# Optimization experiments

Hardware: AMD Instinct MI355X
Metric: run time of the kernel (lower is better)

The kernel has to match this reference:

```python
import jax, jax.numpy as jnp
import numpy as np

_H = jnp.array([[1, 1, 1, 1], [1, -1, 1, -1], [1, 1, -1, -1], [1, -1, -1, 1]], dtype=jnp.float32)
_H2 = _H[jnp.array([1, 0, 2, 3]), :]
_IH = 0.25 * _H[1:3, :]    # inverse Hadamard (H/4), rows 1:3 as in source
_IH2 = 0.25 * _H2[1:3, :]
K = 4  # kernel
S = 2  # stride


def setup_inputs() -> dict:
    key = jax.random.key(0)
    k1, k2, k3 = jax.random.split(key, 3)
    x = jax.random.normal(k1, (32, 64, 56, 56), dtype=jnp.float32)
    weight = jax.random.normal(k2, (128, 64, 4, 4), dtype=jnp.float32) * 0.05
    bias = jax.random.normal(k3, (1, 128, 1, 1), dtype=jnp.float32) * 0.05
    return {"x": x, "weight": weight, "bias": bias}


def reference(x, weight, bias):
    N, C, ih, iw = x.shape
    OC = weight.shape[0]
    nH, nW = ih // S, iw // S  # tiles after stride-2 unfold of the padded input
    xp = jnp.pad(x, ((0, 0), (0, 0), (1, 1), (1, 1)))
    # patches[n,c,h,w,a,b]: a = width-window index, b = height-window index
    # (matches torch x.unfold(3,K,S).unfold(2,K,S) dim ordering)
    patches = jnp.stack(
        [jnp.stack([xp[:, :, bb:bb + 2 * nH:S, aa:aa + 2 * nW:S] for bb in range(K)], axis=-1)
         for aa in range(K)], axis=-2)  # (N,C,nH,nW,K,K)
    # forward Hadamard transforms:  H @ p @ H   and   H2^T @ p @ H2
    T1 = jnp.einsum('ia,nchwab,bj->nchwij', _H, patches, _H)
    T2 = jnp.einsum('ai,nchwab,bj->nchwij', _H2, patches, _H2)
    half = OC // 2
    # elementwise multiply in transform domain + sum over input channels (vectorized over o)
    y1 = jnp.einsum('nchwij,ocij->nohwij', T1, weight[:half])
    y2 = jnp.einsum('nchwij,ocij->nohwij', T2, weight[half:])
    # inverse transform: IH @ y @ IH^T -> 2x2 output tiles
    z1 = jnp.einsum('pi,nohwij,qj->nohwpq', _IH, y1, _IH)
    z2 = jnp.einsum('pi,nohwij,qj->nohwpq', _IH2, y2, _IH2)
    hm = jnp.concatenate([z1, z2], axis=1)  # (N,OC,nH,nW,2,2)
    out = hm.transpose(0, 1, 2, 4, 3, 5).reshape(N, OC, ih, iw)
    return out + bias
```

## Files before the change

### kernel.cpp

```cpp
#include <hip/hip_runtime.h>

typedef __attribute__((ext_vector_type(8))) short bf16x8;
typedef __attribute__((ext_vector_type(4))) float f32x4;
typedef __attribute__((ext_vector_type(2))) float f32x2;
typedef __attribute__((ext_vector_type(2))) unsigned int u32x2;
typedef __attribute__((ext_vector_type(4))) unsigned int u32x4;

#define PITCH     1056
#define AIM_BYTES ((size_t)25088 * PITCH * 2)
#define WEFF_OFF  AIM_BYTES
#define NEED_WS   (AIM_BYTES + (size_t)512 * PITCH * 2)
#define XP_BYTES  (2048 * 3364 * 2)
#define BSTG_OFF  XP_BYTES

static __device__ __forceinline__ unsigned short f2bf(float v) {
    unsigned int u = __builtin_bit_cast(unsigned int, v);
    u += 0x7fffu + ((u >> 16) & 1u);
    return (unsigned short)(u >> 16);
}
static __device__ __forceinline__ void gload_lds16(const void* g, void* l) {
    __builtin_amdgcn_global_load_lds(
        (const __attribute__((address_space(1))) void*)g,
        (__attribute__((address_space(3))) void*)l, 16, 0, 0);
}


__global__ __launch_bounds__(256) void prep3(const float* __restrict__ x,
                                             const float* __restrict__ w,
                                             unsigned char* __restrict__ ws)
{
    int bid = blockIdx.x;
    unsigned short* aim = (unsigned short*)ws;
    if (bid < 896) {
        __shared__ unsigned short lds[256 * 66];
        const int nimg = bid / 28, h = bid - nimg * 28;
        const int tid = threadIdx.x;
        const int wv = tid >> 6, lane = tid & 63;

        unsigned int* l32 = (unsigned int*)lds;
        #pragma unroll
        for (int i = 0; i < 33; ++i)
            l32[tid + i * 256] = 0u;
        __syncthreads();

        const int b_off = (h == 0) ? 1 : 0;
        const int r0 = 2 * h - 1 + b_off;
        const int nrows = 4 - b_off - ((h == 27) ? 1 : 0);
        const int nelem = nrows * 56;
        const int e0 = lane * 4;
        #pragma unroll 4
        for (int i = 0; i < 16; ++i) {
            int c = wv * 16 + i;
            if (e0 < nelem) {
                const float* src = x + ((size_t)(nimg * 64 + c) * 3136 + r0 * 56);
                f32x4 v = *(const f32x4*)(src + e0);
                #pragma unroll
                for (int j = 0; j < 4; ++j) {
                    int e = e0 + j;
                    int rr = e / 56;
                    int col = e - rr * 56;
                    lds[(c * 4 + b_off + rr) * 66 + col + 1] = f2bf(v[j]);
                }
            }
        }
        __syncthreads();

        const int q = tid & 127;
        const int wh = tid >> 7;
        const unsigned int* lr = (const unsigned int*)lds;
        const size_t trow0 = (size_t)nimg * 784 + h * 28;
        const int wa0 = (2 * q) * 33, wa1 = (2 * q + 1) * 33;
        #pragma unroll 7
        for (int it = 0; it < 14; ++it) {
            int wcol = it * 2 + wh;
            unsigned int a0 = lr[wa0 + wcol];
            unsigned int a1 = lr[wa0 + wcol + 1];
            unsigned int b0 = lr[wa1 + wcol];
            unsigned int b1 = lr[wa1 + wcol + 1];
            u32x4 st = {a0, a1, b0, b1};
            *(u32x4*)(aim + (trow0 + wcol) * PITCH + q * 8) = st;
        }
        return;
    }
    int idx = (bid - 896) * 256 + threadIdx.x;
    if (idx >= 128 * 64) return;
    int o = idx >> 6, c = idx & 63;
    const bool v2 = (o >= 64);
    const float Hm[4][4]  = {{1,1,1,1},{1,-1,1,-1},{1,1,-1,-1},{1,-1,-1,1}};
    const float H2m[4][4] = {{1,-1,1,-1},{1,1,1,1},{1,1,-1,-1},{1,-1,-1,1}};
    float wv[4][4];
    #pragma unroll
    for (int i = 0; i < 4; ++i)
        #pragma unroll
        for (int j = 0; j < 4; ++j)
            wv[i][j] = w[((o * 64 + c) * 4 + i) * 4 + j];
    float FA[4][4], FB[4][4], G[2][4];
    #pragma unroll
    for (int a = 0; a < 4; ++a)
        #pragma unroll
        for (int i = 0; i < 4; ++i) {
            FA[a][i] = v2 ? H2m[a][i] : Hm[i][a];
            FB[a][i] = v2 ? H2m[a][i] : Hm[a][i];
        }
    #pragma unroll
    for (int p = 0; p < 2; ++p)
        #pragma unroll
        for (int i = 0; i < 4; ++i)
            G[p][i] = 0.25f * (v2 ? H2m[p + 1][i] : Hm[p + 1][i]);
    unsigned short* weff = (unsigned short*)(ws + WEFF_OFF);
    #pragma unroll
    for (int P = 0; P < 2; ++P)
    #pragma unroll
    for (int Q = 0; Q < 2; ++Q) {
        int nrow = o * 4 + P * 2 + Q;
        #pragma unroll
        for (int b = 0; b < 4; ++b)
        #pragma unroll
        for (int a = 0; a < 4; ++a) {
            float s = 0.f;
            #pragma unroll
            for (int i = 0; i < 4; ++i) {
                float sj = 0.f;
                #pragma unroll
                for (int j = 0; j < 4; ++j)
                    sj += FB[b][j] * G[Q][j] * wv[i][j];
                s += G[P][i] * FA[a][i] * sj;
            }
            weff[(size_t)nrow * PITCH + c * 16 + b * 4 + a] = f2bf(s);
        }
    }
}

__global__ __launch_bounds__(512, 4) void conv_gemm2(
    const unsigned short* __restrict__ aim,
    const unsigned short* __restrict__ weff,
    const float* __restrict__ bias,
    float* __restrict__ out)
{
    __shared__ __align__(16) unsigned char smem[66048];
    unsigned char* Ab0 = smem;
    unsigned char* Bb0 = smem + 32768;
    int* s_obase = (int*)(smem + 65536);

    const int tid  = threadIdx.x;
    const int lane = tid & 63;
    const int l15  = lane & 15;
    const int g    = lane >> 4;
    const int wv   = tid >> 6;
    const int wm   = wv >> 2, wn = wv & 3;
    const int bid  = blockIdx.x;
    const int wid  = (bid & 7) * 98 + (bid >> 3);
    const int tg   = wid >> 2, ng = wid & 3;
    const int t0   = tg << 7;
    const int n0g  = ng << 7;

    if (tid < 128) {
        int t = t0 + tid;
        int nimg = t / 784, rem = t - nimg * 784;
        int h = rem / 28, w = rem - h * 28;
        s_obase[tid] = nimg * 401408 + (2 * h) * 56 + 2 * w;
    }
    __syncthreads();

    const int arow = (wv << 3) + (lane >> 3);
    const int perm = (lane & 7) ^ (lane >> 3);
    const size_t a_src0 = (size_t)(t0 + arow) * PITCH + perm * 8;
    const size_t b_src0 = (size_t)(n0g + arow) * PITCH + perm * 8;

    const int fswz = (l15 & 7) << 4;
    int abase[4], bbase[2];
    #pragma unroll
    for (int fm = 0; fm < 4; ++fm)
        abase[fm] = (wm * 64 + fm * 16 + l15) * 128 + g * 16;
    #pragma unroll
    for (int fn = 0; fn < 2; ++fn)
        bbase[fn] = (wn * 32 + fn * 16 + l15) * 128 + g * 16;

    f32x4 acc[4][2];
    #pragma unroll
    for (int i = 0; i < 4; ++i)
        #pragma unroll
        for (int j = 0; j < 2; ++j)
            acc[i][j] = (f32x4){0.f, 0.f, 0.f, 0.f};

    auto STAGE = [&](int k, int buf) {
        const unsigned short* ga = aim + a_src0 + k * 64;
        const unsigned short* gb = weff + b_src0 + k * 64;
        unsigned char* al = Ab0 + buf * 16384 + wv * 1024;
        unsigned char* bl = Bb0 + buf * 16384 + wv * 1024;
        gload_lds16(ga,              al);
        gload_lds16(ga + 64 * PITCH, al + 8192);
        gload_lds16(gb,              bl);
        gload_lds16(gb + 64 * PITCH, bl + 8192);
    };
    auto MFMA_STEP = [&](int buf) {
        const unsigned char* A = Ab0 + buf * 16384;
        const unsigned char* B = Bb0 + buf * 16384;
        __builtin_amdgcn_s_setprio(1);
        #pragma unroll
        for (int ks = 0; ks < 2; ++ks) {
            bf16x8 af[4], bg[2];
            #pragma unroll
            for (int fm = 0; fm < 4; ++fm)
                af[fm] = *(const bf16x8*)(A + ((abase[fm] | (ks << 6)) ^ fswz));
            #pragma unroll
            for (int fn = 0; fn < 2; ++fn)
                bg[fn] = *(const bf16x8*)(B + ((bbase[fn] | (ks << 6)) ^ fswz));
            #pragma unroll
            for (int fm = 0; fm < 4; ++fm)
                #pragma unroll
                for (int fn = 0; fn < 2; ++fn)
                    acc[fm][fn] = __builtin_amdgcn_mfma_f32_16x16x32_bf16(
                        af[fm], bg[fn], acc[fm][fn], 0, 0, 0);
        }
        __builtin_amdgcn_s_setprio(0);
    };

    STAGE(0, 0);
    asm volatile("s_waitcnt vmcnt(0)" ::: "memory");
    __builtin_amdgcn_s_barrier();
    __builtin_amdgcn_sched_barrier(0);

    #pragma unroll 2
    for (int k = 0; k < 15; ++k) {
        STAGE(k + 1, (k + 1) & 1);
        asm volatile("s_waitcnt vmcnt(4)" ::: "memory");
        __builtin_amdgcn_s_barrier();
        __builtin_amdgcn_sched_barrier(0);
        MFMA_STEP(k & 1);
        __builtin_amdgcn_s_barrier();
        __builtin_amdgcn_sched_barrier(0);
    }
    asm volatile("s_waitcnt vmcnt(0)" ::: "memory");
    __builtin_amdgcn_s_barrier();
    __builtin_amdgcn_sched_barrier(0);
    MFMA_STEP(1);
    __builtin_amdgcn_s_barrier();
    __builtin_amdgcn_sched_barrier(0);

    float bfn[2];
    #pragma unroll
    for (int fn = 0; fn < 2; ++fn)
        bfn[fn] = bias[(n0g + wn * 32 + fn * 16 + l15) >> 2];
    const int ob = s_obase[wm * 64 + lane];
    float* esc = (float*)smem + wv * 1088;

    #pragma unroll
    for (int fn = 0; fn < 2; ++fn) {
        #pragma unroll
        for (int fm = 0; fm < 4; ++fm)
            #pragma unroll
            for (int r = 0; r < 4; ++r)
                esc[(fm * 16 + g * 4 + r) * 17 + l15] = acc[fm][fn][r] + bfn[fn];
        asm volatile("s_waitcnt lgkmcnt(0)" ::: "memory");
        __builtin_amdgcn_sched_barrier(0);
        const int ncb = n0g + wn * 32 + fn * 16;
        #pragma unroll
        for (int jp = 0; jp < 8; ++jp) {
            float v0 = esc[lane * 17 + 2 * jp];
            float v1 = esc[lane * 17 + 2 * jp + 1];
            int n = ncb + 2 * jp;
            int o = n >> 2, P = (n >> 1) & 1;
            f32x2 st = {v0, v1};
            *(f32x2*)(out + ob + o * 3136 + P * 56) = st;
        }
        asm volatile("s_waitcnt lgkmcnt(0)" ::: "memory");
        __builtin_amdgcn_sched_barrier(0);
    }
}

__global__ __launch_bounds__(256) void prep_old(const float* __restrict__ x,
                                                const float* __restrict__ w,
                                                unsigned char* __restrict__ ws)
{
    int bid = blockIdx.x;
    if (bid < 2048) {
        const float* src = x + (size_t)bid * 3136;
        unsigned int* dst = (unsigned int*)ws + (size_t)bid * 1682;
        for (int s = threadIdx.x; s < 1682; s += 256) {
            int r = s / 29, p = s - r * 29;
            float v0 = 0.f, v1 = 0.f;
            if (r >= 1 && r <= 56) {
                const float* row = src + (r - 1) * 56;
                if (p >= 1)  v0 = row[2 * p - 1];
                if (p <= 27) v1 = row[2 * p];
            }
            dst[s] = (unsigned int)f2bf(v0) | ((unsigned int)f2bf(v1) << 16);
        }
        return;
    }
    int idx = (bid - 2048) * 256 + threadIdx.x;
    if (idx >= 128 * 64) return;
    int o = idx >> 6, c = idx & 63;
    const bool v2 = (o >= 64);
    const float Hm[4][4]  = {{1,1,1,1},{1,-1,1,-1},{1,1,-1,-1},{1,-1,-1,1}};
    const float H2m[4][4] = {{1,-1,1,-1},{1,1,1,1},{1,1,-1,-1},{1,-1,-1,1}};
    float wv[4][4];
    #pragma unroll
    for (int i = 0; i < 4; ++i)
        #pragma unroll
        for (int j = 0; j < 4; ++j)
            wv[i][j] = w[((o * 64 + c) * 4 + i) * 4 + j];
    float FA[4][4], FB[4][4], G[2][4];
    #pragma unroll
    for (int a = 0; a < 4; ++a)
        #pragma unroll
        for (int i = 0; i < 4; ++i) {
            FA[a][i] = v2 ? H2m[a][i] : Hm[i][a];
            FB[a][i] = v2 ? H2m[a][i] : Hm[a][i];
        }
    #pragma unroll
    for (int p = 0; p < 2; ++p)
        #pragma unroll
        for (int i = 0; i < 4; ++i)
            G[p][i] = 0.25f * (v2 ? H2m[p + 1][i] : Hm[p + 1][i]);
    unsigned short* weff = (unsigned short*)(ws + BSTG_OFF);
    #pragma unroll
    for (int P = 0; P < 2; ++P)
    #pragma unroll
    for (int Q = 0; Q < 2; ++Q) {
        int nrow = o * 4 + P * 2 + Q;
        #pragma unroll
        for (int b = 0; b < 4; ++b)
        #pragma unroll
        for (int a = 0; a < 4; ++a) {
            float s = 0.f;
            #pragma unroll
            for (int i = 0; i < 4; ++i) {
                float sj = 0.f;
                #pragma unroll
                for (int j = 0; j < 4; ++j)
                    sj += FB[b][j] * G[Q][j] * wv[i][j];
                s += G[P][i] * FA[a][i] * sj;
            }
            weff[(size_t)nrow * 1024 + c * 16 + b * 4 + a] = f2bf(s);
        }
    }
}

__global__ __launch_bounds__(256, 3) void conv_gemm_old(
    const unsigned short* __restrict__ xp,
    const unsigned short* __restrict__ weff,
    const float* __restrict__ bias,
    float* __restrict__ out)
{
    __shared__ __align__(16) unsigned char Abuf[2][16384];
    __shared__ int s_pbase[128];
    __shared__ int s_obase[128];
    const int tid  = threadIdx.x;
    const int lane = tid & 63;
    const int l15  = lane & 15;
    const int g    = lane >> 4;
    const int wv   = tid >> 6;
    const int wm   = wv >> 1, wn = wv & 1;
    const int bid  = blockIdx.x;
    const int wid = (bid & 7) * 98 + (bid >> 3);
    const int tg  = wid >> 2, ng = wid & 3;
    const int t0  = tg << 7;
    const int n0g = ng << 7;
    if (tid < 128) {
        int t = t0 + tid;
        int nimg = t / 784, rem = t - nimg * 784;
        int h = rem / 28, w = rem - h * 28;
        s_pbase[tid] = nimg * 215296 + (2 * h) * 58 + 2 * w;
        s_obase[tid] = nimg * 401408 + (2 * h) * 56 + 2 * w;
    }
    __syncthreads();
    const int t     = tid & 127;
    const int chalf = tid >> 7;
    const int ebase0 = s_pbase[t] + chalf * 6728;
    int wbyte[4];
    #pragma unroll
    for (int q = 0; q < 4; ++q)
        wbyte[q] = (t * 128 + chalf * 64 + q * 16) ^ ((t & 7) << 4);
    const int fswz = (l15 & 7) << 4;
    int abase[4];
    #pragma unroll
    for (int fm = 0; fm < 4; ++fm)
        abase[fm] = (wm * 64 + fm * 16 + l15) * 128 + g * 16;
    const char* bb = (const char*)weff;
    unsigned int boff[4];
    #pragma unroll
    for (int fn = 0; fn < 4; ++fn)
        boff[fn] = (unsigned)((n0g + wn * 64 + fn * 16 + l15) * 2048 + g * 16);
    f32x4 acc[4][4];
    #pragma unroll
    for (int i = 0; i < 4; ++i)
        #pragma unroll
        for (int j = 0; j < 4; ++j)
            acc[i][j] = (f32x4){0.f, 0.f, 0.f, 0.f};
    unsigned int Ar[16];
    bf16x8 bg[8];
    auto GATHER_A = [&](int k) {
        const unsigned short* p = xp + (ebase0 + k * 13456);
        #pragma unroll
        for (int cp = 0; cp < 2; ++cp)
            #pragma unroll
            for (int b = 0; b < 4; ++b) {
                const unsigned short* q = p + cp * 3364 + b * 58;
                Ar[cp * 8 + b * 2]     = *(const unsigned int*)(q);
                Ar[cp * 8 + b * 2 + 1] = *(const unsigned int*)(q + 2);
            }
    };
    auto STAGE_A = [&](int buf) {
        #pragma unroll
        for (int q = 0; q < 4; ++q) {
            u32x4 v = {Ar[q * 4], Ar[q * 4 + 1], Ar[q * 4 + 2], Ar[q * 4 + 3]};
            *(u32x4*)(Abuf[buf] + wbyte[q]) = v;
        }
    };
    auto LOAD_B = [&](int k) {
        const char* q = bb + (unsigned)k * 128u;
        #pragma unroll
        for (int fn = 0; fn < 4; ++fn)
            #pragma unroll
            for (int ks = 0; ks < 2; ++ks)
                bg[fn * 2 + ks] = *(const bf16x8*)(q + boff[fn] + ks * 64);
    };
    auto MFMA_STEP = [&](int buf) {
        const unsigned char* Ab = Abuf[buf];
        __builtin_amdgcn_s_setprio(1);
        #pragma unroll
        for (int ks = 0; ks < 2; ++ks) {
            bf16x8 af[4];
            #pragma unroll
            for (int fm = 0; fm < 4; ++fm)
                af[fm] = *(const bf16x8*)(Ab + ((abase[fm] | (ks << 6)) ^ fswz));
            #pragma unroll
            for (int fm = 0; fm < 4; ++fm)
                #pragma unroll
                for (int fn = 0; fn < 4; ++fn)
                    acc[fm][fn] = __builtin_amdgcn_mfma_f32_16x16x32_bf16(
                        af[fm], bg[fn * 2 + ks], acc[fm][fn], 0, 0, 0);
        }
        __builtin_amdgcn_s_setprio(0);
    };
    GATHER_A(0);
    STAGE_A(0);
    asm volatile("s_waitcnt lgkmcnt(0)" ::: "memory");
    __builtin_amdgcn_s_barrier();
    __builtin_amdgcn_sched_barrier(0);
#define STEP(K, LAST)                                                       \
    do {                                                                    \
        LOAD_B(K);                                                          \
        if (!(LAST)) GATHER_A((K) + 1);                                     \
        MFMA_STEP((K) & 1);                                                 \
        if (!(LAST)) {                                                      \
            STAGE_A(((K) + 1) & 1);                                         \
            asm volatile("s_waitcnt lgkmcnt(0)" ::: "memory");              \
            __builtin_amdgcn_s_barrier();                                   \
            __builtin_amdgcn_sched_barrier(0);                              \
        }                                                                   \
    } while (0)
    STEP(0, 0);  STEP(1, 0);  STEP(2, 0);  STEP(3, 0);
    STEP(4, 0);  STEP(5, 0);  STEP(6, 0);  STEP(7, 0);
    STEP(8, 0);  STEP(9, 0);  STEP(10, 0); STEP(11, 0);
    STEP(12, 0); STEP(13, 0); STEP(14, 0); STEP(15, 1);
#undef STEP
    float bfn[4];
    #pragma unroll
    for (int fn = 0; fn < 4; ++fn)
        bfn[fn] = bias[(n0g + wn * 64 + fn * 16 + l15) >> 2];
    const int ob = s_obase[wm * 64 + lane];
    asm volatile("s_waitcnt lgkmcnt(0)" ::: "memory");
    __builtin_amdgcn_s_barrier();
    __builtin_amdgcn_sched_barrier(0);
    float* esc = (float*)(&Abuf[0][0]) + wv * (64 * 17);
    #pragma unroll
    for (int fn = 0; fn < 4; ++fn) {
        #pragma unroll
        for (int fm = 0; fm < 4; ++fm)
            #pragma unroll
            for (int r = 0; r < 4; ++r)
                esc[(fm * 16 + g * 4 + r) * 17 + l15] = acc[fm][fn][r] + bfn[fn];
        asm volatile("s_waitcnt lgkmcnt(0)" ::: "memory");
        __builtin_amdgcn_sched_barrier(0);
        const int ncb = n0g + wn * 64 + fn * 16;
        #pragma unroll
        for (int jp = 0; jp < 8; ++jp) {
            float v0 = esc[lane * 17 + 2 * jp];
            float v1 = esc[lane * 17 + 2 * jp + 1];
            int n = ncb + 2 * jp;
            int o = n >> 2, P = (n >> 1) & 1;
            f32x2 st = {v0, v1};
            *(f32x2*)(out + ob + o * 3136 + P * 56) = st;
        }
        asm volatile("s_waitcnt lgkmcnt(0)" ::: "memory");
        __builtin_amdgcn_sched_barrier(0);
    }
}

extern "C" void kernel_launch(void* const* d_in, const int* in_sizes, int n_in,
                              void* d_out, int out_size, void* d_ws, size_t ws_size,
                              hipStream_t stream)
{
    const float* x = (const float*)d_in[0];
    const float* w = (const float*)d_in[1];
    const float* b = (const float*)d_in[2];
    float* out = (float*)d_out;
    unsigned char* ws = (unsigned char*)d_ws;

    if (ws_size >= NEED_WS) {
        hipLaunchKernelGGL(prep3, dim3(896 + 32), dim3(256), 0, stream, x, w, ws);
        hipLaunchKernelGGL(conv_gemm2, dim3(784), dim3(512), 0, stream,
                           (const unsigned short*)ws,
                           (const unsigned short*)(ws + WEFF_OFF), b, out);
    } else {
        hipLaunchKernelGGL(prep_old, dim3(2048 + 32), dim3(256), 0, stream, x, w, ws);
        hipLaunchKernelGGL(conv_gemm_old, dim3(784), dim3(256), 0, stream,
                           (const unsigned short*)ws,
                           (const unsigned short*)(ws + BSTG_OFF), b, out);
    }
}
```

Baseline: 61.26 us.

## Replace LDS double-buffered GEMM with direct global-to-register MFMA loads

The GEMM kernel no longer stages A and B tiles through LDS with global_load_lds double buffering. Each wave now loads its bf16 fragments directly from global memory into registers. The block shrinks from 512 to 256 threads, and each wave computes a 64x64 tile instead of 64x32. This removes the LDS traffic and most barriers and raises per-wave register reuse. In exchange, fragment loads within a block are duplicated and served from cache, global load latency is no longer hidden by explicit prefetching, and register pressure rises.

```diff
diff --git a/kernel.cpp b/kernel.cpp
--- a/kernel.cpp
+++ b/kernel.cpp
@@ -3,10 +3,10 @@
 typedef __attribute__((ext_vector_type(8))) short bf16x8;
 typedef __attribute__((ext_vector_type(4))) float f32x4;
 typedef __attribute__((ext_vector_type(2))) float f32x2;
-typedef __attribute__((ext_vector_type(2))) unsigned int u32x2;
 typedef __attribute__((ext_vector_type(4))) unsigned int u32x4;
 
 #define PITCH     1056
+#define PITCHB    2112
 #define AIM_BYTES ((size_t)25088 * PITCH * 2)
 #define WEFF_OFF  AIM_BYTES
 #define NEED_WS   (AIM_BYTES + (size_t)512 * PITCH * 2)
@@ -131,28 +131,26 @@
     }
 }
 
-__global__ __launch_bounds__(512, 4) void conv_gemm2(
-    const unsigned short* __restrict__ aim,
-    const unsigned short* __restrict__ weff,
+__global__ __launch_bounds__(256, 3) void conv_gemm3(
+    const unsigned char* __restrict__ aimb,
+    const unsigned char* __restrict__ weffb,
     const float* __restrict__ bias,
     float* __restrict__ out)
 {
-    __shared__ __align__(16) unsigned char smem[66048];
-    unsigned char* Ab0 = smem;
-    unsigned char* Bb0 = smem + 32768;
-    int* s_obase = (int*)(smem + 65536);
+    __shared__ float esc_s[4 * 1088];
+    __shared__ int s_obase[128];
 
     const int tid  = threadIdx.x;
     const int lane = tid & 63;
     const int l15  = lane & 15;
     const int g    = lane >> 4;
     const int wv   = tid >> 6;
-    const int wm   = wv >> 2, wn = wv & 3;
+    const int wm   = wv >> 1, wn = wv & 1;
     const int bid  = blockIdx.x;
     const int wid  = (bid & 7) * 98 + (bid >> 3);
-    const int tg   = wid >> 2, ng = wid & 3;
+    const int tg   = wid >> 2, ngrp = wid & 3;
     const int t0   = tg << 7;
-    const int n0g  = ng << 7;
+    const int n0g  = ngrp << 7;
 
     if (tid < 128) {
         int t = t0 + tid;
@@ -162,91 +160,56 @@
     }
     __syncthreads();
 
-    const int arow = (wv << 3) + (lane >> 3);
-    const int perm = (lane & 7) ^ (lane >> 3);
-    const size_t a_src0 = (size_t)(t0 + arow) * PITCH + perm * 8;
-    const size_t b_src0 = (size_t)(n0g + arow) * PITCH + perm * 8;
-
-    const int fswz = (l15 & 7) << 4;
-    int abase[4], bbase[2];
+    unsigned int aoff[4], boff[4];
     #pragma unroll
     for (int fm = 0; fm < 4; ++fm)
-        abase[fm] = (wm * 64 + fm * 16 + l15) * 128 + g * 16;
-    #pragma unroll
-    for (int fn = 0; fn < 2; ++fn)
-        bbase[fn] = (wn * 32 + fn * 16 + l15) * 128 + g * 16;
-
-    f32x4 acc[4][2];
+        aoff[fm] = (unsigned)((t0 + wm * 64 + fm * 16 + l15) * PITCHB + g * 16);
+    #pragma unroll
+    for (int fn = 0; fn < 4; ++fn)
+        boff[fn] = (unsigned)((n0g + wn * 64 + fn * 16 + l15) * PITCHB + g * 16);
+
+    f32x4 acc[4][4];
     #pragma unroll
     for (int i = 0; i < 4; ++i)
         #pragma unroll
-        for (int j = 0; j < 2; ++j)
+        for (int j = 0; j < 4; ++j)
             acc[i][j] = (f32x4){0.f, 0.f, 0.f, 0.f};
 
-    auto STAGE = [&](int k, int buf) {
-        const unsigned short* ga = aim + a_src0 + k * 64;
-        const unsigned short* gb = weff + b_src0 + k * 64;
-        unsigned char* al = Ab0 + buf * 16384 + wv * 1024;
-        unsigned char* bl = Bb0 + buf * 16384 + wv * 1024;
-        gload_lds16(ga,              al);
-        gload_lds16(ga + 64 * PITCH, al + 8192);
-        gload_lds16(gb,              bl);
-        gload_lds16(gb + 64 * PITCH, bl + 8192);
-    };
-    auto MFMA_STEP = [&](int buf) {
-        const unsigned char* A = Ab0 + buf * 16384;
-        const unsigned char* B = Bb0 + buf * 16384;
-        __builtin_amdgcn_s_setprio(1);
-        #pragma unroll
-        for (int ks = 0; ks < 2; ++ks) {
-            bf16x8 af[4], bg[2];
-            #pragma unroll
-            for (int fm = 0; fm < 4; ++fm)
-                af[fm] = *(const bf16x8*)(A + ((abase[fm] | (ks << 6)) ^ fswz));
-            #pragma unroll
-            for (int fn = 0; fn < 2; ++fn)
-                bg[fn] = *(const bf16x8*)(B + ((bbase[fn] | (ks << 6)) ^ fswz));
+    #pragma unroll
+    for (int k = 0; k < 16; ++k) {
+        __builtin_amdgcn_s_barrier();
+        __builtin_amdgcn_sched_barrier(0);
+        const int kb = k << 7;
+        bf16x8 af[4][2], bg[4][2];
+        #pragma unroll
+        for (int fm = 0; fm < 4; ++fm)
+            #pragma unroll
+            for (int ks = 0; ks < 2; ++ks)
+                af[fm][ks] = *(const bf16x8*)(aimb + (aoff[fm] + kb + ks * 64));
+        #pragma unroll
+        for (int fn = 0; fn < 4; ++fn)
+            #pragma unroll
+            for (int ks = 0; ks < 2; ++ks)
+                bg[fn][ks] = *(const bf16x8*)(weffb + (boff[fn] + kb + ks * 64));
+        #pragma unroll
+        for (int ks = 0; ks < 2; ++ks)
             #pragma unroll
             for (int fm = 0; fm < 4; ++fm)
                 #pragma unroll
-                for (int fn = 0; fn < 2; ++fn)
+                for (int fn = 0; fn < 4; ++fn)
                     acc[fm][fn] = __builtin_amdgcn_mfma_f32_16x16x32_bf16(
-                        af[fm], bg[fn], acc[fm][fn], 0, 0, 0);
-        }
-        __builtin_amdgcn_s_setprio(0);
-    };
-
-    STAGE(0, 0);
-    asm volatile("s_waitcnt vmcnt(0)" ::: "memory");
-    __builtin_amdgcn_s_barrier();
-    __builtin_amdgcn_sched_barrier(0);
-
-    #pragma unroll 2
-    for (int k = 0; k < 15; ++k) {
-        STAGE(k + 1, (k + 1) & 1);
-        asm volatile("s_waitcnt vmcnt(4)" ::: "memory");
-        __builtin_amdgcn_s_barrier();
-        __builtin_amdgcn_sched_barrier(0);
-        MFMA_STEP(k & 1);
-        __builtin_amdgcn_s_barrier();
-        __builtin_amdgcn_sched_barrier(0);
-    }
-    asm volatile("s_waitcnt vmcnt(0)" ::: "memory");
-    __builtin_amdgcn_s_barrier();
-    __builtin_amdgcn_sched_barrier(0);
-    MFMA_STEP(1);
-    __builtin_amdgcn_s_barrier();
-    __builtin_amdgcn_sched_barrier(0);
-
-    float bfn[2];
-    #pragma unroll
-    for (int fn = 0; fn < 2; ++fn)
-        bfn[fn] = bias[(n0g + wn * 32 + fn * 16 + l15) >> 2];
+                        af[fm][ks], bg[fn][ks], acc[fm][fn], 0, 0, 0);
+    }
+
+    float bfn[4];
+    #pragma unroll
+    for (int fn = 0; fn < 4; ++fn)
+        bfn[fn] = bias[(n0g + wn * 64 + fn * 16 + l15) >> 2];
     const int ob = s_obase[wm * 64 + lane];
-    float* esc = (float*)smem + wv * 1088;
-
-    #pragma unroll
-    for (int fn = 0; fn < 2; ++fn) {
+    float* esc = esc_s + wv * 1088;
+
+    #pragma unroll
+    for (int fn = 0; fn < 4; ++fn) {
         #pragma unroll
         for (int fm = 0; fm < 4; ++fm)
             #pragma unroll
@@ -254,7 +217,7 @@
                 esc[(fm * 16 + g * 4 + r) * 17 + l15] = acc[fm][fn][r] + bfn[fn];
         asm volatile("s_waitcnt lgkmcnt(0)" ::: "memory");
         __builtin_amdgcn_sched_barrier(0);
-        const int ncb = n0g + wn * 32 + fn * 16;
+        const int ncb = n0g + wn * 64 + fn * 16;
         #pragma unroll
         for (int jp = 0; jp < 8; ++jp) {
             float v0 = esc[lane * 17 + 2 * jp];
@@ -502,9 +465,8 @@
 
     if (ws_size >= NEED_WS) {
         hipLaunchKernelGGL(prep3, dim3(896 + 32), dim3(256), 0, stream, x, w, ws);
-        hipLaunchKernelGGL(conv_gemm2, dim3(784), dim3(512), 0, stream,
-                           (const unsigned short*)ws,
-                           (const unsigned short*)(ws + WEFF_OFF), b, out);
+        hipLaunchKernelGGL(conv_gemm3, dim3(784), dim3(256), 0, stream,
+                           ws, ws + WEFF_OFF, b, out);
     } else {
         hipLaunchKernelGGL(prep_old, dim3(2048 + 32), dim3(256), 0, stream, x, w, ws);
         hipLaunchKernelGGL(conv_gemm_old, dim3(784), dim3(256), 0, stream,
```

After: 124.5 us. 103% more time.
